# Performance work log

Measured on AMD Instinct MI355X. Metric: run time of the kernel, lower is better.

The kernel has to match this reference:

```python
import jax, jax.numpy as jnp
import numpy as np

N_NODES = 2048
N_PAIRS = 65536
D = 512
P = 16


def setup_inputs() -> dict:
    key = jax.random.key(0)
    ks = jax.random.split(key, 9)
    scale = 1.0 / np.sqrt(D)
    obj_feats = jax.random.normal(ks[0], (N_NODES, D), dtype=jnp.float32)
    union_feats = jax.random.normal(ks[1], (N_PAIRS, D), dtype=jnp.float32)
    pair_idxs = jax.random.randint(ks[2], (N_PAIRS, 2), 0, N_NODES, dtype=jnp.int64)
    ws_w = jax.random.uniform(ks[3], (D, D), jnp.float32, -scale, scale)
    ws_b = jax.random.uniform(ks[4], (D,), jnp.float32, -scale, scale)
    wo_w = jax.random.uniform(ks[5], (D, D), jnp.float32, -scale, scale)
    wo_b = jax.random.uniform(ks[6], (D,), jnp.float32, -scale, scale)
    w_w = jax.random.uniform(ks[7], (P, D), jnp.float32, -scale, scale)
    w_b = jax.random.uniform(ks[8], (P,), jnp.float32, -scale, scale)
    return {
        'obj_feats': obj_feats, 'union_feats': union_feats, 'pair_idxs': pair_idxs,
        'ws_w': ws_w, 'ws_b': ws_b, 'wo_w': wo_w, 'wo_b': wo_b, 'w_w': w_w, 'w_b': w_b,
    }


def reference(obj_feats, union_feats, pair_idxs, ws_w, ws_b, wo_w, wo_b, w_w, w_b):
    n = obj_feats.shape[0]
    p = w_w.shape[0]
    # node projections: [N, D]
    s = obj_feats @ ws_w.T + ws_b
    o = obj_feats @ wo_w.T + wo_b
    # gather pair features and fuse elementwise product: [E, D]
    prod = s[pair_idxs[:, 0]] * o[pair_idxs[:, 1]] * union_feats
    # project to p attention logits per pair: [E, p]
    atten_f = prod @ w_w.T + w_b
    # scatter into dense [N, N, p]
    atten = jnp.zeros((n, n, p), dtype=obj_feats.dtype)
    atten = atten.at[pair_idxs[:, 0], pair_idxs[:, 1]].add(atten_f)
    # mask diagonal with -1e4 and softmax over axis=1 (incoming nodes)
    atten = atten - jnp.eye(n, dtype=obj_feats.dtype)[:, :, None] * 10000.0
    return jax.nn.softmax(atten, axis=1)
```

## Files before the change

kernel.cpp:

```cpp
#include <hip/hip_runtime.h>
#include <hip/hip_bf16.h>

#define N_NODES 2048
#define N_PAIRS 65536
#define DIM 512
#define NP 16
#define SLOTS 96

typedef __attribute__((ext_vector_type(8))) short s16x8;
typedef __attribute__((ext_vector_type(8))) unsigned short u16x8;
typedef __attribute__((ext_vector_type(4))) float f32x4;

static __device__ __forceinline__ unsigned short f2bf(float x) {
    union { float f; unsigned int u; } v; v.f = x;
    unsigned int r = v.u + 0x7FFFu + ((v.u >> 16) & 1u);
    return (unsigned short)(r >> 16);
}
static __device__ __forceinline__ float bf2f(unsigned short u) {
    union { unsigned int u; float f; } v; v.u = ((unsigned int)u) << 16;
    return v.f;
}
static __device__ __forceinline__ u16x8 pack8(float4 a, float4 b) {
    u16x8 r;
    r[0]=f2bf(a.x); r[1]=f2bf(a.y); r[2]=f2bf(a.z); r[3]=f2bf(a.w);
    r[4]=f2bf(b.x); r[5]=f2bf(b.y); r[6]=f2bf(b.z); r[7]=f2bf(b.w);
    return r;
}

#define GBM 64
#define GBN 64
#define GBK 32
#define GSA 40

__global__ __launch_bounds__(256) void gemm_so(
    const float* __restrict__ A, const float* __restrict__ Ws, const float* __restrict__ bsv,
    const float* __restrict__ Wo, const float* __restrict__ bov,
    unsigned short* __restrict__ Sb, unsigned short* __restrict__ Ob)
{
    __shared__ unsigned short As[GBM*GSA];
    __shared__ unsigned short Bs[GBN*GSA];
    const int tid = threadIdx.x;
    const int m0 = blockIdx.y*GBM, n0 = blockIdx.x*GBN;
    const int ar = tid>>2, ac = (tid&3)*8;
    const float* Arow = A + (size_t)(m0+ar)*DIM + ac;
    const int nrow = n0 + ar;
    const float* Wrow = (nrow < DIM ? Ws + (size_t)nrow*DIM : Wo + (size_t)(nrow-DIM)*DIM) + ac;
    float4 a_r[2], b_r[2];
    a_r[0] = *(const float4*)(Arow);   a_r[1] = *(const float4*)(Arow+4);
    b_r[0] = *(const float4*)(Wrow);   b_r[1] = *(const float4*)(Wrow+4);

    const int lane = tid&63, wid = tid>>6;
    const int wm = (wid>>1)*32, wn = (wid&1)*32;
    const int fr = lane&15, ks8 = (lane>>4)*8;
    f32x4 acc[2][2] = {};
    for (int k0=0; k0<DIM; k0+=GBK) {
        *(u16x8*)&As[ar*GSA+ac] = pack8(a_r[0],a_r[1]);
        *(u16x8*)&Bs[ar*GSA+ac] = pack8(b_r[0],b_r[1]);
        __syncthreads();
        if (k0+GBK < DIM) {
            a_r[0] = *(const float4*)(Arow + k0+GBK);   a_r[1] = *(const float4*)(Arow + k0+GBK + 4);
            b_r[0] = *(const float4*)(Wrow + k0+GBK);   b_r[1] = *(const float4*)(Wrow + k0+GBK + 4);
        }
        s16x8 af[2], bfr[2];
        #pragma unroll
        for (int mi=0;mi<2;++mi) af[mi]  = *(const s16x8*)&As[(wm+mi*16+fr)*GSA + ks8];
        #pragma unroll
        for (int ni=0;ni<2;++ni) bfr[ni] = *(const s16x8*)&Bs[(wn+ni*16+fr)*GSA + ks8];
        #pragma unroll
        for (int mi=0;mi<2;++mi)
            #pragma unroll
            for (int ni=0;ni<2;++ni)
                acc[mi][ni] = __builtin_amdgcn_mfma_f32_16x16x32_bf16(af[mi], bfr[ni], acc[mi][ni], 0,0,0);
        __syncthreads();
    }
    const int rg = lane>>4;
    #pragma unroll
    for (int ni=0;ni<2;++ni) {
        const int n = n0 + wn + ni*16 + fr;
        const float bias = (n < DIM) ? bsv[n] : bov[n-DIM];
        unsigned short* dst = (n < DIM) ? (Sb + n) : (Ob + (n - DIM));
        #pragma unroll
        for (int mi=0;mi<2;++mi) {
            #pragma unroll
            for (int q=0;q<4;++q) {
                const int m = m0 + wm + mi*16 + rg*4 + q;
                dst[(size_t)m*DIM] = f2bf(acc[mi][ni][q] + bias);
            }
        }
    }
}

__global__ __launch_bounds__(256) void pairproj_k(
    const unsigned short* __restrict__ Sb, const unsigned short* __restrict__ Ob,
    const float* __restrict__ U, const int* __restrict__ idx,
    const float* __restrict__ w_w, const float* __restrict__ w_b,
    int* __restrict__ rowcnt, int* __restrict__ rowj, float* __restrict__ rowv)
{
    const int tid = threadIdx.x;
    const int lane = tid & 63, wid = tid >> 6;
    const int fr = lane & 15, ks8 = (lane >> 4) * 8;
    s16x8 wreg[16];
    #pragma unroll
    for (int st = 0; st < 16; ++st) {
        const float4* wp = (const float4*)(w_w + (size_t)fr*DIM + st*32 + ks8);
        u16x8 t = pack8(wp[0], wp[1]);
        wreg[st] = *(s16x8*)&t;
    }
    const float wbv = w_b[fr];

    const int e = blockIdx.x * 64 + wid * 16 + fr;
    const int i = idx[2*e], j = idx[2*e + 1];
    const unsigned short* sp = Sb + (size_t)i * DIM;
    const unsigned short* op = Ob + (size_t)j * DIM;
    const float*          up = U  + (size_t)e * DIM;

    f32x4 acc = {0.f, 0.f, 0.f, 0.f};
    #pragma unroll 4
    for (int st = 0; st < 16; ++st) {
        const int k = st*32 + ks8;
        u16x8 sv = *(const u16x8*)(sp + k);
        u16x8 ov = *(const u16x8*)(op + k);
        float4 u0 = *(const float4*)(up + k);
        float4 u1 = *(const float4*)(up + k + 4);
        float4 p0, p1;
        p0.x = bf2f(sv[0])*bf2f(ov[0])*u0.x;
        p0.y = bf2f(sv[1])*bf2f(ov[1])*u0.y;
        p0.z = bf2f(sv[2])*bf2f(ov[2])*u0.z;
        p0.w = bf2f(sv[3])*bf2f(ov[3])*u0.w;
        p1.x = bf2f(sv[4])*bf2f(ov[4])*u1.x;
        p1.y = bf2f(sv[5])*bf2f(ov[5])*u1.y;
        p1.z = bf2f(sv[6])*bf2f(ov[6])*u1.z;
        p1.w = bf2f(sv[7])*bf2f(ov[7])*u1.w;
        u16x8 pa = pack8(p0, p1);
        acc = __builtin_amdgcn_mfma_f32_16x16x32_bf16(*(s16x8*)&pa, wreg[st], acc, 0,0,0);
    }
    int posv = 0;
    if (lane < 16) {
        posv = atomicAdd(&rowcnt[i], 1);
        if (posv < SLOTS) rowj[i*SLOTS + posv] = j;
    }
    const int rg = lane >> 4;
    #pragma unroll
    for (int q = 0; q < 4; ++q) {
        const int pr = rg*4 + q;
        const int ip = __shfl(i, pr, 64);
        const int pp = __shfl(posv, pr, 64);
        if (pp < SLOTS)
            rowv[((size_t)ip*SLOTS + pp)*NP + fr] = acc[q] + wbv;
    }
}

__global__ __launch_bounds__(256) void softmax_k(
    const int* __restrict__ rowcnt, const int* __restrict__ rowj,
    const float* __restrict__ rowv, float* __restrict__ out)
{
    __shared__ __align__(16) float vals[(SLOTS+2)*NP];
    __shared__ int jcol[SLOTS];
    __shared__ unsigned char deadf[SLOTS];
    __shared__ unsigned char cmap[N_NODES];
    __shared__ float red[16][17];
    __shared__ float mPv[NP], invZv[NP];
    __shared__ int ndv;
    const int r = blockIdx.x;
    const int t = threadIdx.x;
    int c = rowcnt[r];
    if (c > SLOTS) c = SLOTS;

    if (t == 0) ndv = 0;
    for (int n = t; n < N_NODES; n += 256) cmap[n] = (unsigned char)SLOTS;
    for (int a = t; a < c; a += 256) {
        jcol[a] = rowj[r*SLOTS + a];
        deadf[a] = 0;
        const float4* src = (const float4*)(rowv + ((size_t)r*SLOTS + a)*NP);
        float4* dst = (float4*)&vals[a*NP];
        dst[0]=src[0]; dst[1]=src[1]; dst[2]=src[2]; dst[3]=src[3];
    }
    __syncthreads();

    for (int a = t; a < c; a += 256) {
        int j = jcol[a]; int first = a;
        for (int b = 0; b < a; ++b) if (jcol[b] == j) { first = b; break; }
        if (first != a) {
            deadf[a] = 1;
            #pragma unroll
            for (int p = 0; p < NP; ++p) atomicAdd(&vals[first*NP+p], vals[a*NP+p]);
        }
    }
    __syncthreads();
    for (int a = t; a < c; a += 256)
        if (!deadf[a] && jcol[a] != r) atomicAdd(&ndv, 1);
    __syncthreads();

    const int p = t & 15, ch = t >> 4;
    float pm = 0.f;
    for (int a = ch; a < c; a += 16)
        if (!deadf[a] && jcol[a] != r) pm = fmaxf(pm, vals[a*NP+p]);
    red[ch][p] = pm;
    __syncthreads();
    if (t < NP) {
        float m = 0.f;
        #pragma unroll
        for (int k = 0; k < 16; ++k) m = fmaxf(m, red[k][t]);
        mPv[t] = m;
    }
    __syncthreads();
    {
        const float m = mPv[p];
        float ps = 0.f;
        for (int a = ch; a < c; a += 16)
            if (!deadf[a] && jcol[a] != r) ps += __expf(vals[a*NP+p] - m);
        red[ch][p] = ps;
    }
    __syncthreads();
    if (t < NP) {
        float zs = 0.f;
        #pragma unroll
        for (int k = 0; k < 16; ++k) zs += red[k][t];
        const float m = mPv[t];
        const float eb = __expf(-m);
        const float Z = zs + (float)(N_NODES - 1 - ndv) * eb;
        const float iz = 1.0f / Z;
        invZv[t] = iz;
        vals[SLOTS*NP + t] = eb * iz;
        vals[(SLOTS+1)*NP + t] = 0.f;
    }
    __syncthreads();

    for (int a = t; a < c; a += 256) {
        if (!deadf[a] && jcol[a] != r) {
            #pragma unroll
            for (int p2 = 0; p2 < NP; ++p2)
                vals[a*NP+p2] = __expf(vals[a*NP+p2] - mPv[p2]) * invZv[p2];
            cmap[jcol[a]] = (unsigned char)a;
        }
    }
    __syncthreads();
    if (t == 0) cmap[r] = (unsigned char)(SLOTS+1);
    __syncthreads();

    float4* orow = (float4*)(out + (size_t)r * N_NODES * NP);
    const float4* v4 = (const float4*)vals;
    #pragma unroll 8
    for (int n = 0; n < 32; ++n) {
        const int i4 = t + 256*n;
        const int col = i4 >> 2, q = i4 & 3;
        orow[i4] = v4[(int)cmap[col]*4 + q];
    }
}

extern "C" void kernel_launch(void* const* d_in, const int* in_sizes, int n_in,
                              void* d_out, int out_size, void* d_ws, size_t ws_size,
                              hipStream_t stream)
{
    (void)in_sizes; (void)n_in; (void)out_size; (void)ws_size;
    const float* obj  = (const float*)d_in[0];
    const float* uni  = (const float*)d_in[1];
    const int*   idx  = (const int*)  d_in[2];
    const float* ws_w = (const float*)d_in[3];
    const float* ws_b = (const float*)d_in[4];
    const float* wo_w = (const float*)d_in[5];
    const float* wo_b = (const float*)d_in[6];
    const float* w_w  = (const float*)d_in[7];
    const float* w_b  = (const float*)d_in[8];
    float* out = (float*)d_out;

    unsigned short* Sb = (unsigned short*)d_ws;
    unsigned short* Ob = Sb + (size_t)N_NODES * DIM;
    float* rowv  = (float*)(Ob + (size_t)N_NODES * DIM);
    int* rowj    = (int*)(rowv + (size_t)N_NODES * SLOTS * NP);
    int* rowcnt  = rowj + (size_t)N_NODES * SLOTS;

    hipMemsetAsync(rowcnt, 0, N_NODES * sizeof(int), stream);
    gemm_so<<<dim3(1024/GBN, N_NODES/GBM), 256, 0, stream>>>(obj, ws_w, ws_b, wo_w, wo_b, Sb, Ob);
    pairproj_k<<<N_PAIRS/64, 256, 0, stream>>>(Sb, Ob, uni, idx, w_w, w_b, rowcnt, rowj, rowv);
    softmax_k<<<N_NODES, 256, 0, stream>>>(rowcnt, rowj, rowv, out);
}
```

Baseline: 149.2 us.

## Fuse pair projection into per-row softmax kernel with edge routing pass

Adds a small routing kernel that buckets edge ids by source row, then fuses the pair-product MFMA projection into the per-row softmax kernel. Each row block computes its edges' logits directly into shared memory, reusing the row's S vector, which removes the rowv intermediate write/read and one kernel. The cost is more shared memory per block (~66KB for P), lower occupancy, and serialized per-edge gathers within a wave, with row load imbalance.

```diff
diff --git a/kernel.cpp b/kernel.cpp
--- a/kernel.cpp
+++ b/kernel.cpp
@@ -6,6 +6,7 @@
 #define DIM 512
 #define NP 16
 #define SLOTS 96
+#define SP 520
 
 typedef __attribute__((ext_vector_type(8))) short s16x8;
 typedef __attribute__((ext_vector_type(8))) unsigned short u16x8;
@@ -90,95 +91,99 @@
     }
 }
 
-__global__ __launch_bounds__(256) void pairproj_k(
+__global__ __launch_bounds__(256) void route_k(
+    const int* __restrict__ idx, int* __restrict__ rowcnt, int* __restrict__ rowj)
+{
+    const int e = blockIdx.x * 256 + threadIdx.x;
+    const int i = idx[2*e];
+    const int pos = atomicAdd(&rowcnt[i], 1);
+    if (pos < SLOTS) rowj[i*SLOTS + pos] = e;
+}
+
+__global__ __launch_bounds__(256) void fused_sm(
     const unsigned short* __restrict__ Sb, const unsigned short* __restrict__ Ob,
     const float* __restrict__ U, const int* __restrict__ idx,
     const float* __restrict__ w_w, const float* __restrict__ w_b,
-    int* __restrict__ rowcnt, int* __restrict__ rowj, float* __restrict__ rowv)
-{
-    const int tid = threadIdx.x;
-    const int lane = tid & 63, wid = tid >> 6;
-    const int fr = lane & 15, ks8 = (lane >> 4) * 8;
-    s16x8 wreg[16];
-    #pragma unroll
-    for (int st = 0; st < 16; ++st) {
-        const float4* wp = (const float4*)(w_w + (size_t)fr*DIM + st*32 + ks8);
-        u16x8 t = pack8(wp[0], wp[1]);
-        wreg[st] = *(s16x8*)&t;
-    }
-    const float wbv = w_b[fr];
-
-    const int e = blockIdx.x * 64 + wid * 16 + fr;
-    const int i = idx[2*e], j = idx[2*e + 1];
-    const unsigned short* sp = Sb + (size_t)i * DIM;
-    const unsigned short* op = Ob + (size_t)j * DIM;
-    const float*          up = U  + (size_t)e * DIM;
-
-    f32x4 acc = {0.f, 0.f, 0.f, 0.f};
-    #pragma unroll 4
-    for (int st = 0; st < 16; ++st) {
-        const int k = st*32 + ks8;
-        u16x8 sv = *(const u16x8*)(sp + k);
-        u16x8 ov = *(const u16x8*)(op + k);
-        float4 u0 = *(const float4*)(up + k);
-        float4 u1 = *(const float4*)(up + k + 4);
-        float4 p0, p1;
-        p0.x = bf2f(sv[0])*bf2f(ov[0])*u0.x;
-        p0.y = bf2f(sv[1])*bf2f(ov[1])*u0.y;
-        p0.z = bf2f(sv[2])*bf2f(ov[2])*u0.z;
-        p0.w = bf2f(sv[3])*bf2f(ov[3])*u0.w;
-        p1.x = bf2f(sv[4])*bf2f(ov[4])*u1.x;
-        p1.y = bf2f(sv[5])*bf2f(ov[5])*u1.y;
-        p1.z = bf2f(sv[6])*bf2f(ov[6])*u1.z;
-        p1.w = bf2f(sv[7])*bf2f(ov[7])*u1.w;
-        u16x8 pa = pack8(p0, p1);
-        acc = __builtin_amdgcn_mfma_f32_16x16x32_bf16(*(s16x8*)&pa, wreg[st], acc, 0,0,0);
-    }
-    int posv = 0;
-    if (lane < 16) {
-        posv = atomicAdd(&rowcnt[i], 1);
-        if (posv < SLOTS) rowj[i*SLOTS + posv] = j;
-    }
-    const int rg = lane >> 4;
-    #pragma unroll
-    for (int q = 0; q < 4; ++q) {
-        const int pr = rg*4 + q;
-        const int ip = __shfl(i, pr, 64);
-        const int pp = __shfl(posv, pr, 64);
-        if (pp < SLOTS)
-            rowv[((size_t)ip*SLOTS + pp)*NP + fr] = acc[q] + wbv;
-    }
-}
-
-__global__ __launch_bounds__(256) void softmax_k(
     const int* __restrict__ rowcnt, const int* __restrict__ rowj,
-    const float* __restrict__ rowv, float* __restrict__ out)
-{
+    float* __restrict__ out)
+{
+    __shared__ __align__(16) unsigned short P[4*16*SP];
     __shared__ __align__(16) float vals[(SLOTS+2)*NP];
+    __shared__ int elds[SLOTS];
     __shared__ int jcol[SLOTS];
     __shared__ unsigned char deadf[SLOTS];
     __shared__ unsigned char cmap[N_NODES];
     __shared__ float red[16][17];
     __shared__ float mPv[NP], invZv[NP];
     __shared__ int ndv;
+
     const int r = blockIdx.x;
     const int t = threadIdx.x;
+    const int lane = t & 63, wid = t >> 6;
+    const int fr = lane & 15, ks8 = (lane >> 4) * 8;
+
+    s16x8 wreg[16];
+    #pragma unroll
+    for (int st = 0; st < 16; ++st) {
+        const float4* wp = (const float4*)(w_w + (size_t)fr*DIM + st*32 + ks8);
+        u16x8 tm = pack8(wp[0], wp[1]);
+        wreg[st] = *(s16x8*)&tm;
+    }
+    const float wbv = w_b[fr];
+
     int c = rowcnt[r];
     if (c > SLOTS) c = SLOTS;
 
     if (t == 0) ndv = 0;
     for (int n = t; n < N_NODES; n += 256) cmap[n] = (unsigned char)SLOTS;
     for (int a = t; a < c; a += 256) {
-        jcol[a] = rowj[r*SLOTS + a];
+        const int e = rowj[r*SLOTS + a];
+        elds[a] = e;
+        jcol[a] = idx[2*e + 1];
         deadf[a] = 0;
-        const float4* src = (const float4*)(rowv + ((size_t)r*SLOTS + a)*NP);
-        float4* dst = (float4*)&vals[a*NP];
-        dst[0]=src[0]; dst[1]=src[1]; dst[2]=src[2]; dst[3]=src[3];
+    }
+    __syncthreads();
+
+    const u16x8 sv = *(const u16x8*)(Sb + (size_t)r*DIM + lane*8);
+
+    unsigned short* Pw = &P[wid*16*SP];
+    for (int a0 = wid*16; a0 < c; a0 += 64) {
+        const int nb = (c - a0 < 16) ? (c - a0) : 16;
+        for (int s8 = 0; s8 < nb; ++s8) {
+            const int e = elds[a0 + s8];
+            const int j = jcol[a0 + s8];
+            const u16x8 ov = *(const u16x8*)(Ob + (size_t)j*DIM + lane*8);
+            const float4* up = (const float4*)(U + (size_t)e*DIM + lane*8);
+            const float4 u0 = up[0], u1 = up[1];
+            float4 p0, p1;
+            p0.x = bf2f(sv[0])*bf2f(ov[0])*u0.x;
+            p0.y = bf2f(sv[1])*bf2f(ov[1])*u0.y;
+            p0.z = bf2f(sv[2])*bf2f(ov[2])*u0.z;
+            p0.w = bf2f(sv[3])*bf2f(ov[3])*u0.w;
+            p1.x = bf2f(sv[4])*bf2f(ov[4])*u1.x;
+            p1.y = bf2f(sv[5])*bf2f(ov[5])*u1.y;
+            p1.z = bf2f(sv[6])*bf2f(ov[6])*u1.z;
+            p1.w = bf2f(sv[7])*bf2f(ov[7])*u1.w;
+            *(u16x8*)&Pw[s8*SP + lane*8] = pack8(p0, p1);
+        }
+        f32x4 acc = {0.f, 0.f, 0.f, 0.f};
+        #pragma unroll
+        for (int st = 0; st < 16; ++st) {
+            s16x8 af = *(const s16x8*)&Pw[fr*SP + st*32 + ks8];
+            acc = __builtin_amdgcn_mfma_f32_16x16x32_bf16(af, wreg[st], acc, 0,0,0);
+        }
+        const int rg = lane >> 4;
+        #pragma unroll
+        for (int q = 0; q < 4; ++q) {
+            const int sa = rg*4 + q;
+            if (sa < nb) vals[(a0 + sa)*NP + fr] = acc[q] + wbv;
+        }
     }
     __syncthreads();
 
     for (int a = t; a < c; a += 256) {
-        int j = jcol[a]; int first = a;
+        const int j = jcol[a];
+        int first = a;
         for (int b = 0; b < a; ++b) if (jcol[b] == j) { first = b; break; }
         if (first != a) {
             deadf[a] = 1;
@@ -266,12 +271,11 @@
 
     unsigned short* Sb = (unsigned short*)d_ws;
     unsigned short* Ob = Sb + (size_t)N_NODES * DIM;
-    float* rowv  = (float*)(Ob + (size_t)N_NODES * DIM);
-    int* rowj    = (int*)(rowv + (size_t)N_NODES * SLOTS * NP);
-    int* rowcnt  = rowj + (size_t)N_NODES * SLOTS;
+    int* rowj   = (int*)(Ob + (size_t)N_NODES * DIM);
+    int* rowcnt = rowj + (size_t)N_NODES * SLOTS;
 
     hipMemsetAsync(rowcnt, 0, N_NODES * sizeof(int), stream);
+    route_k<<<N_PAIRS/256, 256, 0, stream>>>(idx, rowcnt, rowj);
     gemm_so<<<dim3(1024/GBN, N_NODES/GBM), 256, 0, stream>>>(obj, ws_w, ws_b, wo_w, wo_b, Sb, Ob);
-    pairproj_k<<<N_PAIRS/64, 256, 0, stream>>>(Sb, Ob, uni, idx, w_w, w_b, rowcnt, rowj, rowv);
-    softmax_k<<<N_NODES, 256, 0, stream>>>(rowcnt, rowj, rowv, out);
-}
+    fused_sm<<<N_NODES, 256, 0, stream>>>(Sb, Ob, uni, idx, w_w, w_b, rowcnt, rowj, out);
+}
```

Result: slower. 165.9 us (+11.2%).
